# Optimization experiments

Hardware: AMD Instinct MI355X
Metric: run time of the kernel (lower is better)

## Reference

```python
import jax, jax.numpy as jnp
import numpy as np

NUM_HEADS = 16
NUM_GROUPS = 4
EPS = 1e-6


def _rope_tables(seq_len, head_dim):
    inv_freq = 1.0 / (10000.0 ** (jnp.arange(0, head_dim, 2, dtype=jnp.float32) / head_dim))
    t = jnp.arange(seq_len, dtype=jnp.float32)
    freqs = jnp.outer(t, inv_freq)  # [s, hd//2]
    return jnp.sin(freqs), jnp.cos(freqs)


def _apply_rope(x, sin, cos):
    # x: [b, s, h, hd]; sin/cos: [s, hd//2] -> broadcast over batch and heads
    sin = sin[None, :, None, :]
    cos = cos[None, :, None, :]
    x1 = x[..., ::2]
    x2 = x[..., 1::2]
    out1 = x1 * cos - x2 * sin
    out2 = x1 * sin + x2 * cos
    return jnp.stack([out1, out2], axis=-1).reshape(x.shape).astype(x.dtype)


def _rmsnorm(x, scale):
    var = jnp.mean(jnp.square(x), axis=-1, keepdims=True)
    return x * jax.lax.rsqrt(var + EPS) * scale


def setup_inputs() -> dict:
    key = jax.random.key(0)
    b, s, d = 16, 512, 2048
    hd = d // NUM_HEADS
    g = NUM_GROUPS
    ks = jax.random.split(key, 9)
    std = 0.02
    return {
        "x": jax.random.normal(ks[0], (b, s, d), dtype=jnp.float32),
        "Wq": jax.random.normal(ks[1], (d, d), dtype=jnp.float32) * std,
        "bq": jnp.zeros((d,), dtype=jnp.float32),
        "Wk": jax.random.normal(ks[2], (d, g * hd), dtype=jnp.float32) * std,
        "bk": jnp.zeros((g * hd,), dtype=jnp.float32),
        "Wv": jax.random.normal(ks[3], (d, g * hd), dtype=jnp.float32) * std,
        "bv": jnp.zeros((g * hd,), dtype=jnp.float32),
        "Wo": jax.random.normal(ks[4], (d, d), dtype=jnp.float32) * std,
        "bo": jnp.zeros((d,), dtype=jnp.float32),
        "q_norm_scale": jnp.ones((hd,), dtype=jnp.float32),
        "k_norm_scale": jnp.ones((hd,), dtype=jnp.float32),
    }


def reference(x, Wq, bq, Wk, bk, Wv, bv, Wo, bo, q_norm_scale, k_norm_scale):
    b, s, d = x.shape
    H, G = NUM_HEADS, NUM_GROUPS
    hd = d // H
    P = H // G  # queries per kv group
    inv_sqrt_hd = hd ** (-0.5)

    q = (x @ Wq + bq).reshape(b, s, H, hd)
    k = (x @ Wk + bk).reshape(b, s, G, hd)
    v = (x @ Wv + bv).reshape(b, s, G, hd)

    q = _rmsnorm(q, q_norm_scale)
    k = _rmsnorm(k, k_norm_scale)

    sin, cos = _rope_tables(s, hd)
    q = _apply_rope(q, sin, cos) * inv_sqrt_hd  # module pre-scales q
    k = _apply_rope(k, sin, cos)

    # GQA attention with causal mask; dot_product_attention applies an
    # additional 1/sqrt(hd) scale on top of the module's pre-scaling.
    qg = q.reshape(b, s, G, P, hd)
    logits = jnp.einsum("bsgph,btgh->bgpst", qg, k) * inv_sqrt_hd
    causal = jnp.tril(jnp.ones((s, s), dtype=bool))
    logits = jnp.where(causal[None, None, None, :, :], logits, jnp.finfo(logits.dtype).min)
    attn = jax.nn.softmax(logits, axis=-1)
    out = jnp.einsum("bgpst,btgh->bsgph", attn, v).reshape(b, s, d)
    return out @ Wo + bo
```

## Files before the change

### kernel.cpp

```cpp
#include <hip/hip_runtime.h>
#include <stdint.h>

typedef __attribute__((ext_vector_type(4))) float floatx4;
typedef __attribute__((ext_vector_type(16))) float floatx16;
typedef __attribute__((ext_vector_type(8))) short short8;

#define BB 16
#define SS 512
#define DD 2048
#define HH_ 16
#define HD 128
#define GG 4
#define MM (BB*SS)
#define NQKV 3072

__device__ __forceinline__ unsigned short f2bf(float f){
  unsigned u = __builtin_bit_cast(unsigned, f);
  u += 0x7fffu + ((u >> 16) & 1u);
  return (unsigned short)(u >> 16);
}
__device__ __forceinline__ float bf2f_lo(unsigned d){
  return __builtin_bit_cast(float, d << 16);
}
__device__ __forceinline__ float bf2f_hi(unsigned d){
  return __builtin_bit_cast(float, d & 0xffff0000u);
}

__device__ __forceinline__ void async_copy16(const void* g, void* l){
  __builtin_amdgcn_global_load_lds((const __attribute__((address_space(1))) unsigned*)g,
                                   (__attribute__((address_space(3))) unsigned*)l,
                                   16, 0, 0);
}

#define PB_CVT   16384
#define PB_TRQ   (PB_CVT + 4096)
#define PB_TRK   (PB_TRQ + 1024)
#define PB_TRV   (PB_TRK + 1024)
#define PB_TRO   (PB_TRV + 4096)
#define PB_ALL   (PB_TRO + 12)

__global__ __launch_bounds__(256) void prep_kernel(
    const float* __restrict__ x,
    const float* __restrict__ Wq, const float* __restrict__ Wk,
    const float* __restrict__ Wv, const float* __restrict__ Wo,
    const float* __restrict__ bq, const float* __restrict__ bk,
    const float* __restrict__ bv,
    unsigned short* __restrict__ xb, unsigned short* __restrict__ WqkvT,
    unsigned short* __restrict__ WoT, float* __restrict__ bqkv)
{
  __shared__ float tile[32][33];
  const int bid = blockIdx.x, tid = threadIdx.x;

  if (bid < PB_CVT) {
    const int i = bid * 256 + tid;
    float4 f = ((const float4*)x)[i];
    ushort4 o;
    o.x = f2bf(f.x); o.y = f2bf(f.y); o.z = f2bf(f.z); o.w = f2bf(f.w);
    ((ushort4*)xb)[i] = o;
    return;
  }
  if (bid < PB_TRO) {
    const float* src; unsigned short* dst; int R, C, b2;
    if (bid < PB_TRQ)      { src = Wq; dst = WqkvT;                          R = 2048; C = 2048; b2 = bid - PB_CVT; }
    else if (bid < PB_TRK) { src = Wk; dst = WqkvT + (size_t)2048 * 2048;    R = 2048; C = 512;  b2 = bid - PB_TRQ; }
    else if (bid < PB_TRV) { src = Wv; dst = WqkvT + (size_t)2560 * 2048;    R = 2048; C = 512;  b2 = bid - PB_TRK; }
    else                   { src = Wo; dst = WoT;                            R = 2048; C = 2048; b2 = bid - PB_TRV; }
    const int nbx = C >> 5;
    const int c0 = (b2 % nbx) * 32, r0 = (b2 / nbx) * 32;
    const int tx = tid & 31, ty = tid >> 5;
    #pragma unroll
    for (int j = 0; j < 32; j += 8)
      tile[ty + j][tx] = src[(size_t)(r0 + ty + j) * C + (c0 + tx)];
    __syncthreads();
    #pragma unroll
    for (int j = 0; j < 32; j += 8)
      dst[(size_t)(c0 + ty + j) * R + (r0 + tx)] = f2bf(tile[tx][ty + j]);
    return;
  }
  {
    const int i = (bid - PB_TRO) * 256 + tid;
    if (i < NQKV)
      bqkv[i] = (i < 2048) ? bq[i] : (i < 2560 ? bk[i - 2048] : bv[i - 2560]);
  }
}

template<bool OUT_BF16>
__global__ __launch_bounds__(256) void gemm_bt_kernel(
    const unsigned short* __restrict__ A,
    const unsigned short* __restrict__ Bt,
    void* __restrict__ Cout,
    const float* __restrict__ bias,
    int M, int N, int K, int ldc)
{
  __shared__ unsigned short sA[128 * 64];
  __shared__ unsigned short sB[128 * 64];
  const int tid  = threadIdx.x;
  const int wave = tid >> 6;
  const int lane = tid & 63;
  const int m0 = blockIdx.y * 128;
  const int n0 = blockIdx.x * 128;
  const int wm = (wave >> 1) * 64;
  const int wn = (wave & 1) * 64;

  floatx16 acc[2][2];
  #pragma unroll
  for (int i = 0; i < 2; i++)
    #pragma unroll
    for (int j = 0; j < 2; j++)
      #pragma unroll
      for (int r = 0; r < 16; r++) acc[i][j][r] = 0.f;

  const int sglog = (lane & 7) ^ ((lane >> 3) & 7);
  const unsigned short* gA = A  + (size_t)(m0 + 32 * wave + (lane >> 3)) * K + sglog * 8;
  const unsigned short* gB = Bt + (size_t)(n0 + 32 * wave + (lane >> 3)) * K + sglog * 8;
  unsigned short* lA = &sA[32 * wave * 64];
  unsigned short* lB = &sB[32 * wave * 64];

  for (int k0 = 0; k0 < K; k0 += 64) {
    #pragma unroll
    for (int c = 0; c < 4; ++c) {
      async_copy16(gA + (size_t)c * 8 * K + k0, lA + c * 512);
      async_copy16(gB + (size_t)c * 8 * K + k0, lB + c * 512);
    }
    __syncthreads();

    #pragma unroll
    for (int kh = 0; kh < 4; ++kh) {
      const int slot = (kh * 2 + (lane >> 5)) ^ (lane & 7);
      short8 aF[2], bF[2];
      #pragma unroll
      for (int i = 0; i < 2; ++i)
        aF[i] = *(const short8*)(&sA[(wm + i * 32 + (lane & 31)) * 64 + slot * 8]);
      #pragma unroll
      for (int j = 0; j < 2; ++j)
        bF[j] = *(const short8*)(&sB[(wn + j * 32 + (lane & 31)) * 64 + slot * 8]);
      #pragma unroll
      for (int i = 0; i < 2; ++i)
        #pragma unroll
        for (int j = 0; j < 2; ++j)
          acc[i][j] = __builtin_amdgcn_mfma_f32_32x32x16_bf16(aF[i], bF[j], acc[i][j], 0, 0, 0);
    }
    __syncthreads();
  }

  const int cc = lane & 31;
  const int rb = 4 * (lane >> 5);
  #pragma unroll
  for (int j = 0; j < 2; j++) {
    const int col = n0 + wn + j * 32 + cc;
    const float bval = bias[col];
    #pragma unroll
    for (int i = 0; i < 2; i++) {
      #pragma unroll
      for (int reg = 0; reg < 16; reg++) {
        const int row = m0 + wm + i * 32 + (reg & 3) + 8 * (reg >> 2) + rb;
        const float v = acc[i][j][reg] + bval;
        if (OUT_BF16)
          ((unsigned short*)Cout)[(size_t)row * ldc + col] = f2bf(v);
        else
          ((float*)Cout)[(size_t)row * ldc + col] = v;
      }
    }
  }
}

__global__ __launch_bounds__(256) void norm_vtr_kernel(
    unsigned short* __restrict__ qkv,
    const float* __restrict__ qs, const float* __restrict__ ks,
    unsigned short* __restrict__ vt)
{
  __shared__ unsigned short tileV[32][34];
  const int bid = blockIdx.x, tid = threadIdx.x;

  if (bid < 40960) {
    const int wave = tid >> 6, lane = tid & 63;
    const int gw  = bid * 4 + wave;
    const int row = gw / 20;
    const int hh  = gw % 20;
    const bool isq = hh < 16;

    unsigned* p = (unsigned*)(qkv + (size_t)row * NQKV + hh * 128) + lane;
    unsigned d = *p;
    float x1 = bf2f_lo(d), x2 = bf2f_hi(d);

    float ss = x1 * x1 + x2 * x2;
    #pragma unroll
    for (int off = 32; off; off >>= 1) ss += __shfl_xor(ss, off, 64);
    const float r = rsqrtf(ss * (1.f / 128.f) + 1e-6f);

    const float2 sc = ((const float2*)(isq ? qs : ks))[lane];
    float n1 = x1 * r * sc.x;
    float n2 = x2 * r * sc.y;

    const float t = (float)(row & (SS - 1));
    const float freq = __expf((float)lane * (-2.f / 128.f) * 9.21034037197618f);
    float sn, cs;
    __sincosf(t * freq, &sn, &cs);
    float o1 = n1 * cs - n2 * sn;
    float o2 = n1 * sn + n2 * cs;
    if (isq) { o1 *= (1.f / 128.f); o2 *= (1.f / 128.f); }

    *p = (unsigned)f2bf(o1) | ((unsigned)f2bf(o2) << 16);
    return;
  }
  {
    const int b2 = bid - 40960;
    const int hd0 = (b2 & 3) * 32, t0 = ((b2 >> 2) & 15) * 32, bg = b2 >> 6;
    const int tx = tid & 31, ty = tid >> 5;
    const int b = bg >> 2, g = bg & 3;
    const unsigned short* src = qkv + (size_t)b * SS * NQKV + 2560 + g * HD;
    #pragma unroll
    for (int j = 0; j < 32; j += 8)
      tileV[ty + j][tx] = src[(size_t)(t0 + ty + j) * NQKV + hd0 + tx];
    __syncthreads();
    unsigned short* dst = vt + (size_t)bg * HD * SS;
    #pragma unroll
    for (int j = 0; j < 32; j += 8)
      dst[(size_t)(hd0 + ty + j) * SS + t0 + tx] = tileV[tx][ty + j];
  }
}

__global__ __launch_bounds__(256, 4) void fattn_kernel(
    const unsigned short* __restrict__ qkv,
    const unsigned short* __restrict__ vtb,
    unsigned short* __restrict__ aout)
{
  __shared__ unsigned short sK[64 * 128];
  __shared__ unsigned short sV[128 * 64];
  __shared__ unsigned short sP[4][16 * 64];

  const int lane = threadIdx.x & 63, wave = threadIdx.x >> 6;
  const int quad = lane >> 4, col = lane & 15;
  const int idx = blockIdx.x;
  const int qb = 7 - (idx >> 8);
  const int bh = idx & 255;
  const int b = bh >> 4, h = bh & 15, g = h >> 2;

  const int qrow = qb * 64 + wave * 16 + col;
  const unsigned short* qg = qkv + ((size_t)(b * SS + qrow)) * NQKV + h * HD + quad * 8;
  short8 qf[4];
  #pragma unroll
  for (int c = 0; c < 4; ++c) qf[c] = *(const short8*)(qg + c * 32);

  const unsigned short* kg = qkv + (size_t)b * SS * NQKV + 2048 + g * HD;
  const unsigned short* vg = vtb + ((size_t)(b * GG + g)) * HD * SS;

  floatx4 acc_o[8];
  #pragma unroll
  for (int i = 0; i < 8; ++i) acc_o[i] = (floatx4){0.f, 0.f, 0.f, 0.f};
  float m[4] = {-INFINITY, -INFINITY, -INFINITY, -INFINITY};
  float l[4] = {0.f, 0.f, 0.f, 0.f};

  for (int kt = 0; kt <= qb; ++kt) {
    const int t0 = kt * 64;
    #pragma unroll
    for (int c = 0; c < 4; ++c) {
      const int ci = c * 4 + wave;
      { const int r  = ci * 4 + (lane >> 4);
        const int gl = (lane & 15) ^ (r & 15);
        async_copy16(kg + (size_t)(t0 + r) * NQKV + gl * 8, &sK[ci * 512]); }
      { const int r  = ci * 8 + (lane >> 3);
        const int gl = (lane & 7) ^ (r & 7);
        async_copy16(vg + (size_t)r * SS + t0 + gl * 8, &sV[ci * 512]); }
    }
    __syncthreads();

    floatx4 sc[4];
    #pragma unroll
    for (int s = 0; s < 4; ++s) sc[s] = (floatx4){0.f, 0.f, 0.f, 0.f};
    #pragma unroll
    for (int s = 0; s < 4; ++s) {
      const int trow = s * 16 + col;
      #pragma unroll
      for (int c = 0; c < 4; ++c) {
        const int p = (c * 4 + quad) ^ (trow & 15);
        const short8 kf = *(const short8*)(&sK[trow * 128 + p * 8]);
        sc[s] = __builtin_amdgcn_mfma_f32_16x16x32_bf16(qf[c], kf, sc[s], 0, 0, 0);
      }
    }

    if (kt == qb) {
      #pragma unroll
      for (int s = 0; s < 4; ++s)
        #pragma unroll
        for (int r = 0; r < 4; ++r)
          if (s * 16 + col > wave * 16 + quad * 4 + r) sc[s][r] = -1e30f;
    }

    float mx[4], alpha[4], lsum[4];
    #pragma unroll
    for (int r = 0; r < 4; ++r) {
      mx[r] = fmaxf(fmaxf(sc[0][r], sc[1][r]), fmaxf(sc[2][r], sc[3][r]));
      #pragma unroll
      for (int off = 8; off; off >>= 1) mx[r] = fmaxf(mx[r], __shfl_xor(mx[r], off, 16));
      mx[r] = fmaxf(mx[r], m[r]);
      alpha[r] = __expf(m[r] - mx[r]);
      m[r] = mx[r];
      lsum[r] = 0.f;
    }
    #pragma unroll
    for (int s = 0; s < 4; ++s)
      #pragma unroll
      for (int r = 0; r < 4; ++r) {
        const float p = __expf(sc[s][r] - m[r]);
        lsum[r] += p;
        const int row = quad * 4 + r;
        const int slot = (s * 2 + (col >> 3)) ^ (row & 7);
        sP[wave][row * 64 + slot * 8 + (col & 7)] = f2bf(p);
      }
    #pragma unroll
    for (int r = 0; r < 4; ++r) {
      #pragma unroll
      for (int off = 8; off; off >>= 1) lsum[r] += __shfl_xor(lsum[r], off, 16);
      l[r] = l[r] * alpha[r] + lsum[r];
    }
    #pragma unroll
    for (int n = 0; n < 8; ++n)
      #pragma unroll
      for (int r = 0; r < 4; ++r) acc_o[n][r] *= alpha[r];

    __asm__ volatile("s_waitcnt lgkmcnt(0)" ::: "memory");

    short8 pf[2];
    #pragma unroll
    for (int kc = 0; kc < 2; ++kc)
      pf[kc] = *(const short8*)(&sP[wave][col * 64 + ((kc * 4 + quad) ^ (col & 7)) * 8]);
    #pragma unroll
    for (int n = 0; n < 8; ++n) {
      const int hdrow = n * 16 + col;
      #pragma unroll
      for (int kc = 0; kc < 2; ++kc) {
        const int p = (kc * 4 + quad) ^ (hdrow & 7);
        const short8 vf = *(const short8*)(&sV[hdrow * 64 + p * 8]);
        acc_o[n] = __builtin_amdgcn_mfma_f32_16x16x32_bf16(pf[kc], vf, acc_o[n], 0, 0, 0);
      }
    }
    __syncthreads();
  }

  float inv[4];
  #pragma unroll
  for (int r = 0; r < 4; ++r) inv[r] = 1.f / l[r];
  unsigned short* ob = aout + ((size_t)(b * SS + qb * 64 + wave * 16)) * DD + h * HD;
  #pragma unroll
  for (int n = 0; n < 8; ++n)
    #pragma unroll
    for (int r = 0; r < 4; ++r)
      ob[(size_t)(quad * 4 + r) * DD + n * 16 + col] = f2bf(acc_o[n][r] * inv[r]);
}

extern "C" void kernel_launch(void* const* d_in, const int* in_sizes, int n_in,
                              void* d_out, int out_size, void* d_ws, size_t ws_size,
                              hipStream_t stream) {
  const float* x   = (const float*)d_in[0];
  const float* Wq  = (const float*)d_in[1];
  const float* bq  = (const float*)d_in[2];
  const float* Wk  = (const float*)d_in[3];
  const float* bk  = (const float*)d_in[4];
  const float* Wv  = (const float*)d_in[5];
  const float* bv  = (const float*)d_in[6];
  const float* Wo  = (const float*)d_in[7];
  const float* bo  = (const float*)d_in[8];
  const float* qns = (const float*)d_in[9];
  const float* kns = (const float*)d_in[10];

  char* ws = (char*)d_ws;
  unsigned short* xb    = (unsigned short*)(ws);
  unsigned short* vtb   = (unsigned short*)(ws);
  unsigned short* WqkvT = (unsigned short*)(ws + 33554432);
  unsigned short* WoT   = (unsigned short*)(ws + 46137344);
  float*          bqkv  = (float*)         (ws + 54525952);
  unsigned short* qkv   = (unsigned short*)(ws + 54538240);
  unsigned short* aout  = (unsigned short*)(ws + 104869888);

  prep_kernel<<<PB_ALL, 256, 0, stream>>>(x, Wq, Wk, Wv, Wo, bq, bk, bv,
                                          xb, WqkvT, WoT, bqkv);
  gemm_bt_kernel<true><<<dim3(24, 64), 256, 0, stream>>>(xb, WqkvT, qkv, bqkv,
                                                         MM, NQKV, DD, NQKV);
  norm_vtr_kernel<<<45056, 256, 0, stream>>>(qkv, qns, kns, vtb);
  fattn_kernel<<<2048, 256, 0, stream>>>(qkv, vtb, aout);
  gemm_bt_kernel<false><<<dim3(16, 64), 256, 0, stream>>>(aout, WoT, d_out, bo,
                                                          MM, DD, DD, DD);
  (void)in_sizes; (void)n_in; (void)out_size; (void)ws_size;
}
```

Before: 433.0 us.

## Replace GEMM with 256x256-tile double-buffered pipelined MFMA kernel

Replaces the 128x128 single-buffered GEMM with a 256x256-tile, 8-wave kernel. It double-buffers the async global-to-LDS copies across K steps, interleaves LDS fragment loads with 16x16x32 MFMA quadrants under explicit waitcnt, barriers and setprio, and remaps block IDs so neighbouring blocks share a chunk of the grid. The goal is to hide global memory latency and cut per-FLOP load traffic in the two projection GEMMs. The trade-offs are 64KB of LDS per block, heavy register pressure, fewer blocks (384 and 256) that may underfill the CUs, and hand-tuned synchronisation that is fragile.

```diff
diff --git a/kernel.cpp b/kernel.cpp
--- a/kernel.cpp
+++ b/kernel.cpp
@@ -85,80 +85,145 @@
 }
 
 template<bool OUT_BF16>
-__global__ __launch_bounds__(256) void gemm_bt_kernel(
+__global__ __launch_bounds__(512, 2) void gemm256_kernel(
     const unsigned short* __restrict__ A,
     const unsigned short* __restrict__ Bt,
     void* __restrict__ Cout,
     const float* __restrict__ bias,
-    int M, int N, int K, int ldc)
+    int N, int K, int ldc)
 {
-  __shared__ unsigned short sA[128 * 64];
-  __shared__ unsigned short sB[128 * 64];
+  __shared__ unsigned short sA[4 * 128 * 64];
+  __shared__ unsigned short sB[4 * 128 * 64];
+
   const int tid  = threadIdx.x;
-  const int wave = tid >> 6;
-  const int lane = tid & 63;
-  const int m0 = blockIdx.y * 128;
-  const int n0 = blockIdx.x * 128;
-  const int wm = (wave >> 1) * 64;
-  const int wn = (wave & 1) * 64;
-
-  floatx16 acc[2][2];
-  #pragma unroll
-  for (int i = 0; i < 2; i++)
-    #pragma unroll
-    for (int j = 0; j < 2; j++)
-      #pragma unroll
-      for (int r = 0; r < 16; r++) acc[i][j][r] = 0.f;
-
-  const int sglog = (lane & 7) ^ ((lane >> 3) & 7);
-  const unsigned short* gA = A  + (size_t)(m0 + 32 * wave + (lane >> 3)) * K + sglog * 8;
-  const unsigned short* gB = Bt + (size_t)(n0 + 32 * wave + (lane >> 3)) * K + sglog * 8;
-  unsigned short* lA = &sA[32 * wave * 64];
-  unsigned short* lB = &sB[32 * wave * 64];
-
-  for (int k0 = 0; k0 < K; k0 += 64) {
-    #pragma unroll
-    for (int c = 0; c < 4; ++c) {
-      async_copy16(gA + (size_t)c * 8 * K + k0, lA + c * 512);
-      async_copy16(gB + (size_t)c * 8 * K + k0, lB + c * 512);
-    }
-    __syncthreads();
-
-    #pragma unroll
-    for (int kh = 0; kh < 4; ++kh) {
-      const int slot = (kh * 2 + (lane >> 5)) ^ (lane & 7);
-      short8 aF[2], bF[2];
-      #pragma unroll
-      for (int i = 0; i < 2; ++i)
-        aF[i] = *(const short8*)(&sA[(wm + i * 32 + (lane & 31)) * 64 + slot * 8]);
-      #pragma unroll
-      for (int j = 0; j < 2; ++j)
-        bF[j] = *(const short8*)(&sB[(wn + j * 32 + (lane & 31)) * 64 + slot * 8]);
-      #pragma unroll
-      for (int i = 0; i < 2; ++i)
-        #pragma unroll
-        for (int j = 0; j < 2; ++j)
-          acc[i][j] = __builtin_amdgcn_mfma_f32_32x32x16_bf16(aF[i], bF[j], acc[i][j], 0, 0, 0);
-    }
-    __syncthreads();
-  }
-
-  const int cc = lane & 31;
-  const int rb = 4 * (lane >> 5);
-  #pragma unroll
-  for (int j = 0; j < 2; j++) {
-    const int col = n0 + wn + j * 32 + cc;
+  const int wave = tid >> 6, lane = tid & 63;
+  const int wm = wave >> 2, wn = wave & 3;
+  const int l15 = lane & 15, l7 = lane & 7, q4 = lane >> 4;
+
+  const int nbn = N >> 8;
+  const int cpx = gridDim.x >> 3;
+  const int bid = (blockIdx.x & 7) * cpx + (blockIdx.x >> 3);
+  const int m0 = (bid / nbn) * 256;
+  const int n0 = (bid % nbn) * 256;
+
+  const int rowOff = wave * 8 + (lane >> 3);
+  const int glog   = l7 ^ ((lane >> 3) & 7);
+  const unsigned short* gA = A  + (size_t)(m0 + rowOff) * K + glog * 8;
+  const unsigned short* gB = Bt + (size_t)(n0 + rowOff) * K + glog * 8;
+
+#define STAGE_A(j, tt) do { \
+    unsigned short* d_ = &sA[(2 * ((tt) & 1) + (j)) * 8192 + wave * 512]; \
+    const unsigned short* s_ = gA + (size_t)((j) * 128) * K + (tt) * 64; \
+    async_copy16(s_, d_); \
+    async_copy16(s_ + (size_t)64 * K, d_ + 4096); } while (0)
+#define STAGE_B(j, tt) do { \
+    unsigned short* d_ = &sB[(2 * ((tt) & 1) + (j)) * 8192 + wave * 512]; \
+    const unsigned short* s_ = gB + (size_t)((j) * 128) * K + (tt) * 64; \
+    async_copy16(s_, d_); \
+    async_copy16(s_ + (size_t)64 * K, d_ + 4096); } while (0)
+
+  STAGE_B(0, 0); STAGE_B(1, 0); STAGE_A(0, 0); STAGE_A(1, 0);
+  STAGE_B(0, 1); STAGE_B(1, 1); STAGE_A(0, 1);
+
+  floatx4 acc[8][4];
+  #pragma unroll
+  for (int i = 0; i < 8; ++i)
+    #pragma unroll
+    for (int j = 0; j < 4; ++j)
+      acc[i][j] = (floatx4){0.f, 0.f, 0.f, 0.f};
+
+  asm volatile("s_waitcnt vmcnt(6)" ::: "memory");
+  __builtin_amdgcn_s_barrier();
+
+  short8 aF[4][2], bF[4][2];
+  const int NT = K >> 6;
+
+  const unsigned short* pA = &sA[l15 * 64];
+  const unsigned short* pB = &sB[((wn & 1) * 64 + l15) * 64];
+  const int g0 = ((0 + q4) ^ l7) * 8;
+  const int g1 = ((4 + q4) ^ l7) * 8;
+
+#define LDA_(fa_, rb_, sa_) do { \
+    aF[fa_][0] = *(const short8*)(pA + (sa_) * 8192 + ((rb_) + (fa_) * 16) * 64 + g0); \
+    aF[fa_][1] = *(const short8*)(pA + (sa_) * 8192 + ((rb_) + (fa_) * 16) * 64 + g1); } while (0)
+#define LDB_(fb_, sb_) do { \
+    bF[fb_][0] = *(const short8*)(pB + (sb_) * 8192 + (fb_) * 16 * 64 + g0); \
+    bF[fb_][1] = *(const short8*)(pB + (sb_) * 8192 + (fb_) * 16 * 64 + g1); } while (0)
+#define MFMA_Q(fa0, fb0) \
+    _Pragma("unroll") \
+    for (int fa = 0; fa < 4; ++fa) { \
+      _Pragma("unroll") \
+      for (int fb = 0; fb < 2; ++fb) { \
+        acc[(fa0)+fa][(fb0)+fb] = __builtin_amdgcn_mfma_f32_16x16x32_bf16(aF[fa][0], bF[(fb0)+fb][0], acc[(fa0)+fa][(fb0)+fb], 0, 0, 0); \
+        acc[(fa0)+fa][(fb0)+fb] = __builtin_amdgcn_mfma_f32_16x16x32_bf16(aF[fa][1], bF[(fb0)+fb][1], acc[(fa0)+fa][(fb0)+fb], 0, 0, 0); \
+      } \
+    }
+
+  #pragma unroll 1
+  for (int t = 0; t < NT; ++t) {
+    const int sa = 2 * (t & 1) + wm;
+    const int sb = 2 * (t & 1) + (wn >> 1);
+    LDA_(0, 0, sa); LDA_(1, 0, sa); LDA_(2, 0, sa); LDA_(3, 0, sa);
+    LDB_(0, sb); LDB_(1, sb);
+    if (t + 1 < NT) STAGE_A(1, t + 1);
+    __builtin_amdgcn_s_barrier();
+    asm volatile("s_waitcnt lgkmcnt(0)" ::: "memory");
+    __builtin_amdgcn_sched_barrier(0);
+    __builtin_amdgcn_s_setprio(1);
+    MFMA_Q(0, 0);
+    __builtin_amdgcn_s_setprio(0);
+    __builtin_amdgcn_s_barrier();
+    LDB_(2, sb); LDB_(3, sb);
+    if (t + 2 < NT) STAGE_B(0, t + 2);
+    __builtin_amdgcn_s_barrier();
+    asm volatile("s_waitcnt lgkmcnt(0)" ::: "memory");
+    __builtin_amdgcn_sched_barrier(0);
+    __builtin_amdgcn_s_setprio(1);
+    MFMA_Q(0, 2);
+    __builtin_amdgcn_s_setprio(0);
+    __builtin_amdgcn_s_barrier();
+    LDA_(0, 64, sa); LDA_(1, 64, sa); LDA_(2, 64, sa); LDA_(3, 64, sa);
+    if (t + 2 < NT) STAGE_B(1, t + 2);
+    __builtin_amdgcn_s_barrier();
+    asm volatile("s_waitcnt lgkmcnt(0)" ::: "memory");
+    __builtin_amdgcn_sched_barrier(0);
+    __builtin_amdgcn_s_setprio(1);
+    MFMA_Q(4, 0);
+    __builtin_amdgcn_s_setprio(0);
+    __builtin_amdgcn_s_barrier();
+    if (t + 2 < NT) {
+      STAGE_A(0, t + 2);
+      asm volatile("s_waitcnt vmcnt(6)" ::: "memory");
+    } else if (t + 1 < NT) {
+      asm volatile("s_waitcnt vmcnt(0)" ::: "memory");
+    }
+    __builtin_amdgcn_s_barrier();
+    __builtin_amdgcn_s_setprio(1);
+    MFMA_Q(4, 2);
+    __builtin_amdgcn_s_setprio(0);
+    __builtin_amdgcn_s_barrier();
+  }
+#undef STAGE_A
+#undef STAGE_B
+#undef LDA_
+#undef LDB_
+#undef MFMA_Q
+
+  const int r4 = q4 * 4;
+  #pragma unroll
+  for (int fb = 0; fb < 4; ++fb) {
+    const int col = n0 + wn * 64 + fb * 16 + l15;
     const float bval = bias[col];
     #pragma unroll
-    for (int i = 0; i < 2; i++) {
-      #pragma unroll
-      for (int reg = 0; reg < 16; reg++) {
-        const int row = m0 + wm + i * 32 + (reg & 3) + 8 * (reg >> 2) + rb;
-        const float v = acc[i][j][reg] + bval;
+    for (int fa = 0; fa < 8; ++fa) {
+      const size_t rowb = (size_t)(m0 + wm * 128 + fa * 16 + r4);
+      #pragma unroll
+      for (int r = 0; r < 4; ++r) {
+        const float v = acc[fa][fb][r] + bval;
         if (OUT_BF16)
-          ((unsigned short*)Cout)[(size_t)row * ldc + col] = f2bf(v);
+          ((unsigned short*)Cout)[(rowb + r) * ldc + col] = f2bf(v);
         else
-          ((float*)Cout)[(size_t)row * ldc + col] = v;
+          ((float*)Cout)[(rowb + r) * ldc + col] = v;
       }
     }
   }
@@ -375,11 +440,11 @@
 
   prep_kernel<<<PB_ALL, 256, 0, stream>>>(x, Wq, Wk, Wv, Wo, bq, bk, bv,
                                           xb, WqkvT, WoT, bqkv);
-  gemm_bt_kernel<true><<<dim3(24, 64), 256, 0, stream>>>(xb, WqkvT, qkv, bqkv,
-                                                         MM, NQKV, DD, NQKV);
+  gemm256_kernel<true><<<384, 512, 0, stream>>>(xb, WqkvT, qkv, bqkv,
+                                                NQKV, DD, NQKV);
   norm_vtr_kernel<<<45056, 256, 0, stream>>>(qkv, qns, kns, vtb);
   fattn_kernel<<<2048, 256, 0, stream>>>(qkv, vtb, aout);
-  gemm_bt_kernel<false><<<dim3(16, 64), 256, 0, stream>>>(aout, WoT, d_out, bo,
-                                                          MM, DD, DD, DD);
+  gemm256_kernel<false><<<256, 512, 0, stream>>>(aout, WoT, d_out, bo,
+                                                 DD, DD, DD);
   (void)in_sizes; (void)n_in; (void)out_size; (void)ws_size;
 }
```

Result: no change. 436.3 us (+0.7%).

## Fuse Q norm/RoPE into attention, double-buffer KV, lazy rescale, 128-row blocks

Applied to the files above, without the earlier changes.

Moves the Q RMSNorm and RoPE out of the standalone norm kernel into the attention kernel's Q-load prologue, so the norm kernel now only handles K and the V transpose. This drops one read-modify-write pass over Q. The attention kernel goes to 512 threads with 128 query rows per block, double-buffers the K/V shared tiles with async copies, and raises MFMA priority around the matmul loops. It also skips the online-softmax rescale unless the running max grows by more than 8, trading a larger LDS footprint and some bf16 precision headroom for fewer syncs and fewer multiplies.

```diff
diff --git a/kernel.cpp b/kernel.cpp
--- a/kernel.cpp
+++ b/kernel.cpp
@@ -164,22 +164,21 @@
   }
 }
 
-__global__ __launch_bounds__(256) void norm_vtr_kernel(
+__global__ __launch_bounds__(256) void knorm_vtr_kernel(
     unsigned short* __restrict__ qkv,
-    const float* __restrict__ qs, const float* __restrict__ ks,
+    const float* __restrict__ ks,
     unsigned short* __restrict__ vt)
 {
   __shared__ unsigned short tileV[32][34];
   const int bid = blockIdx.x, tid = threadIdx.x;
 
-  if (bid < 40960) {
+  if (bid < 8192) {
     const int wave = tid >> 6, lane = tid & 63;
     const int gw  = bid * 4 + wave;
-    const int row = gw / 20;
-    const int hh  = gw % 20;
-    const bool isq = hh < 16;
-
-    unsigned* p = (unsigned*)(qkv + (size_t)row * NQKV + hh * 128) + lane;
+    const int row = gw >> 2;
+    const int kh  = gw & 3;
+
+    unsigned* p = (unsigned*)(qkv + (size_t)row * NQKV + 2048 + kh * 128) + lane;
     unsigned d = *p;
     float x1 = bf2f_lo(d), x2 = bf2f_hi(d);
 
@@ -188,7 +187,7 @@
     for (int off = 32; off; off >>= 1) ss += __shfl_xor(ss, off, 64);
     const float r = rsqrtf(ss * (1.f / 128.f) + 1e-6f);
 
-    const float2 sc = ((const float2*)(isq ? qs : ks))[lane];
+    const float2 sc = ((const float2*)ks)[lane];
     float n1 = x1 * r * sc.x;
     float n2 = x2 * r * sc.y;
 
@@ -198,13 +197,12 @@
     __sincosf(t * freq, &sn, &cs);
     float o1 = n1 * cs - n2 * sn;
     float o2 = n1 * sn + n2 * cs;
-    if (isq) { o1 *= (1.f / 128.f); o2 *= (1.f / 128.f); }
 
     *p = (unsigned)f2bf(o1) | ((unsigned)f2bf(o2) << 16);
     return;
   }
   {
-    const int b2 = bid - 40960;
+    const int b2 = bid - 8192;
     const int hd0 = (b2 & 3) * 32, t0 = ((b2 >> 2) & 15) * 32, bg = b2 >> 6;
     const int tx = tid & 31, ty = tid >> 5;
     const int b = bg >> 2, g = bg & 3;
@@ -220,27 +218,62 @@
   }
 }
 
-__global__ __launch_bounds__(256, 4) void fattn_kernel(
+__global__ __launch_bounds__(512, 4) void fattn_kernel(
     const unsigned short* __restrict__ qkv,
     const unsigned short* __restrict__ vtb,
+    const float* __restrict__ qns,
     unsigned short* __restrict__ aout)
 {
-  __shared__ unsigned short sK[64 * 128];
-  __shared__ unsigned short sV[128 * 64];
-  __shared__ unsigned short sP[4][16 * 64];
+  __shared__ unsigned short sK[2][64 * 128];
+  __shared__ unsigned short sV[2][128 * 64];
+  __shared__ unsigned short sP[8][16 * 64];
 
   const int lane = threadIdx.x & 63, wave = threadIdx.x >> 6;
   const int quad = lane >> 4, col = lane & 15;
   const int idx = blockIdx.x;
-  const int qb = 7 - (idx >> 8);
+  const int qb = (0x1203 >> ((idx >> 8) * 4)) & 0xF;
   const int bh = idx & 255;
   const int b = bh >> 4, h = bh & 15, g = h >> 2;
 
-  const int qrow = qb * 64 + wave * 16 + col;
+  const int qrow = qb * 128 + wave * 16 + col;
   const unsigned short* qg = qkv + ((size_t)(b * SS + qrow)) * NQKV + h * HD + quad * 8;
+
+  uint4 qraw[4];
+  #pragma unroll
+  for (int c = 0; c < 4; ++c) qraw[c] = *(const uint4*)(qg + c * 32);
+  float ssq = 0.f;
+  #pragma unroll
+  for (int c = 0; c < 4; ++c)
+    #pragma unroll
+    for (int u = 0; u < 4; ++u) {
+      const unsigned d = ((const unsigned*)&qraw[c])[u];
+      const float x1 = bf2f_lo(d), x2 = bf2f_hi(d);
+      ssq += x1 * x1 + x2 * x2;
+    }
+  ssq += __shfl_xor(ssq, 16, 64);
+  ssq += __shfl_xor(ssq, 32, 64);
+  const float rms = rsqrtf(ssq * (1.f / 128.f) + 1e-6f);
+
   short8 qf[4];
   #pragma unroll
-  for (int c = 0; c < 4; ++c) qf[c] = *(const short8*)(qg + c * 32);
+  for (int c = 0; c < 4; ++c) {
+    uint4 outp;
+    #pragma unroll
+    for (int u = 0; u < 4; ++u) {
+      const unsigned d = ((const unsigned*)&qraw[c])[u];
+      const int fi = c * 16 + quad * 4 + u;
+      const float2 sc2 = ((const float2*)qns)[fi];
+      const float freq = __expf((float)fi * (-2.f / 128.f) * 9.21034037197618f);
+      float sn, cs;
+      __sincosf((float)qrow * freq, &sn, &cs);
+      const float n1 = bf2f_lo(d) * rms * sc2.x;
+      const float n2 = bf2f_hi(d) * rms * sc2.y;
+      const float o1 = (n1 * cs - n2 * sn) * (1.f / 128.f);
+      const float o2 = (n1 * sn + n2 * cs) * (1.f / 128.f);
+      ((unsigned*)&outp)[u] = (unsigned)f2bf(o1) | ((unsigned)f2bf(o2) << 16);
+    }
+    qf[c] = __builtin_bit_cast(short8, outp);
+  }
 
   const unsigned short* kg = qkv + (size_t)b * SS * NQKV + 2048 + g * HD;
   const unsigned short* vg = vtb + ((size_t)(b * GG + g)) * HD * SS;
@@ -251,53 +284,77 @@
   float m[4] = {-INFINITY, -INFINITY, -INFINITY, -INFINITY};
   float l[4] = {0.f, 0.f, 0.f, 0.f};
 
-  for (int kt = 0; kt <= qb; ++kt) {
-    const int t0 = kt * 64;
-    #pragma unroll
-    for (int c = 0; c < 4; ++c) {
-      const int ci = c * 4 + wave;
-      { const int r  = ci * 4 + (lane >> 4);
-        const int gl = (lane & 15) ^ (r & 15);
-        async_copy16(kg + (size_t)(t0 + r) * NQKV + gl * 8, &sK[ci * 512]); }
-      { const int r  = ci * 8 + (lane >> 3);
-        const int gl = (lane & 7) ^ (r & 7);
-        async_copy16(vg + (size_t)r * SS + t0 + gl * 8, &sV[ci * 512]); }
-    }
+#define STAGE_KV(kt_, bf_) do { \
+    const int t0_ = (kt_) * 64; \
+    _Pragma("unroll") \
+    for (int c = 0; c < 2; ++c) { \
+      const int ci = c * 8 + wave; \
+      { const int r_  = ci * 4 + (lane >> 4); \
+        const int gl_ = (lane & 15) ^ (r_ & 15); \
+        async_copy16(kg + (size_t)(t0_ + r_) * NQKV + gl_ * 8, &sK[bf_][ci * 512]); } \
+      { const int r_  = ci * 8 + (lane >> 3); \
+        const int gl_ = (lane & 7) ^ (r_ & 7); \
+        async_copy16(vg + (size_t)r_ * SS + t0_ + gl_ * 8, &sV[bf_][ci * 512]); } \
+    } } while (0)
+
+  const int nkt = 2 * qb + 2;
+  STAGE_KV(0, 0);
+
+  for (int kt = 0; kt < nkt; ++kt) {
+    const int buf = kt & 1;
     __syncthreads();
+    if (kt + 1 < nkt) STAGE_KV(kt + 1, buf ^ 1);
+
+    if (kt * 64 > qb * 128 + wave * 16 + 15) continue;
 
     floatx4 sc[4];
     #pragma unroll
     for (int s = 0; s < 4; ++s) sc[s] = (floatx4){0.f, 0.f, 0.f, 0.f};
+    __builtin_amdgcn_s_setprio(1);
     #pragma unroll
     for (int s = 0; s < 4; ++s) {
       const int trow = s * 16 + col;
       #pragma unroll
       for (int c = 0; c < 4; ++c) {
         const int p = (c * 4 + quad) ^ (trow & 15);
-        const short8 kf = *(const short8*)(&sK[trow * 128 + p * 8]);
+        const short8 kf = *(const short8*)(&sK[buf][trow * 128 + p * 8]);
         sc[s] = __builtin_amdgcn_mfma_f32_16x16x32_bf16(qf[c], kf, sc[s], 0, 0, 0);
       }
     }
-
-    if (kt == qb) {
+    __builtin_amdgcn_s_setprio(0);
+
+    if (kt >= 2 * qb) {
       #pragma unroll
       for (int s = 0; s < 4; ++s)
         #pragma unroll
         for (int r = 0; r < 4; ++r)
-          if (s * 16 + col > wave * 16 + quad * 4 + r) sc[s][r] = -1e30f;
-    }
-
-    float mx[4], alpha[4], lsum[4];
+          if (kt * 64 + s * 16 + col > qb * 128 + wave * 16 + quad * 4 + r)
+            sc[s][r] = -1e30f;
+    }
+
+    float pm[4];
     #pragma unroll
     for (int r = 0; r < 4; ++r) {
-      mx[r] = fmaxf(fmaxf(sc[0][r], sc[1][r]), fmaxf(sc[2][r], sc[3][r]));
-      #pragma unroll
-      for (int off = 8; off; off >>= 1) mx[r] = fmaxf(mx[r], __shfl_xor(mx[r], off, 16));
-      mx[r] = fmaxf(mx[r], m[r]);
-      alpha[r] = __expf(m[r] - mx[r]);
-      m[r] = mx[r];
-      lsum[r] = 0.f;
-    }
+      pm[r] = fmaxf(fmaxf(sc[0][r], sc[1][r]), fmaxf(sc[2][r], sc[3][r]));
+      #pragma unroll
+      for (int off = 8; off; off >>= 1) pm[r] = fmaxf(pm[r], __shfl_xor(pm[r], off, 16));
+    }
+    const bool keep = (pm[0] <= m[0] + 8.f) && (pm[1] <= m[1] + 8.f) &&
+                      (pm[2] <= m[2] + 8.f) && (pm[3] <= m[3] + 8.f) &&
+                      (m[0] > -1e30f);
+    if (!__all(keep)) {
+      #pragma unroll
+      for (int r = 0; r < 4; ++r) {
+        const float mx = fmaxf(pm[r], m[r]);
+        const float al = __expf(m[r] - mx);
+        m[r] = mx;
+        l[r] *= al;
+        #pragma unroll
+        for (int n = 0; n < 8; ++n) acc_o[n][r] *= al;
+      }
+    }
+
+    float lsum[4] = {0.f, 0.f, 0.f, 0.f};
     #pragma unroll
     for (int s = 0; s < 4; ++s)
       #pragma unroll
@@ -312,36 +369,32 @@
     for (int r = 0; r < 4; ++r) {
       #pragma unroll
       for (int off = 8; off; off >>= 1) lsum[r] += __shfl_xor(lsum[r], off, 16);
-      l[r] = l[r] * alpha[r] + lsum[r];
-    }
-    #pragma unroll
-    for (int n = 0; n < 8; ++n)
-      #pragma unroll
-      for (int r = 0; r < 4; ++r) acc_o[n][r] *= alpha[r];
-
-    __asm__ volatile("s_waitcnt lgkmcnt(0)" ::: "memory");
+      l[r] += lsum[r];
+    }
 
     short8 pf[2];
     #pragma unroll
     for (int kc = 0; kc < 2; ++kc)
       pf[kc] = *(const short8*)(&sP[wave][col * 64 + ((kc * 4 + quad) ^ (col & 7)) * 8]);
+    __builtin_amdgcn_s_setprio(1);
     #pragma unroll
     for (int n = 0; n < 8; ++n) {
       const int hdrow = n * 16 + col;
       #pragma unroll
       for (int kc = 0; kc < 2; ++kc) {
         const int p = (kc * 4 + quad) ^ (hdrow & 7);
-        const short8 vf = *(const short8*)(&sV[hdrow * 64 + p * 8]);
+        const short8 vf = *(const short8*)(&sV[buf][hdrow * 64 + p * 8]);
         acc_o[n] = __builtin_amdgcn_mfma_f32_16x16x32_bf16(pf[kc], vf, acc_o[n], 0, 0, 0);
       }
     }
-    __syncthreads();
-  }
+    __builtin_amdgcn_s_setprio(0);
+  }
+#undef STAGE_KV
 
   float inv[4];
   #pragma unroll
   for (int r = 0; r < 4; ++r) inv[r] = 1.f / l[r];
-  unsigned short* ob = aout + ((size_t)(b * SS + qb * 64 + wave * 16)) * DD + h * HD;
+  unsigned short* ob = aout + ((size_t)(b * SS + qb * 128 + wave * 16)) * DD + h * HD;
   #pragma unroll
   for (int n = 0; n < 8; ++n)
     #pragma unroll
@@ -377,8 +430,8 @@
                                           xb, WqkvT, WoT, bqkv);
   gemm_bt_kernel<true><<<dim3(24, 64), 256, 0, stream>>>(xb, WqkvT, qkv, bqkv,
                                                          MM, NQKV, DD, NQKV);
-  norm_vtr_kernel<<<45056, 256, 0, stream>>>(qkv, qns, kns, vtb);
-  fattn_kernel<<<2048, 256, 0, stream>>>(qkv, vtb, aout);
+  knorm_vtr_kernel<<<12288, 256, 0, stream>>>(qkv, kns, vtb);
+  fattn_kernel<<<1024, 512, 0, stream>>>(qkv, vtb, qns, aout);
   gemm_bt_kernel<false><<<dim3(16, 64), 256, 0, stream>>>(aout, WoT, d_out, bo,
                                                           MM, DD, DD, DD);
   (void)in_sizes; (void)n_in; (void)out_size; (void)ws_size;
```

After: 410.4 us. 1.06x faster.
